# Performance work log

Hardware: AMD Instinct MI355X
Metric: run time of the kernel (lower is better)

Reference implementation:

```python
import jax, jax.numpy as jnp
import numpy as np

N = 100_000            # nodes
E = 1_600_000          # edges per metapath
IN = 256               # input features
HEADS, DIM = 8, 16     # heads * dim = hidden_channels
HIDDEN = HEADS * DIM   # 128
OUT = 4                # classes
NEG_SLOPE = 0.2


def setup_inputs() -> dict:
    key = jax.random.key(0)
    ks = jax.random.split(key, 16)
    s = 1.0 / np.sqrt(HIDDEN)
    return {
        "x": jax.random.normal(ks[0], (N, IN), jnp.float32),
        "edge_index0": jax.random.randint(ks[1], (2, E), 0, N, jnp.int64),
        "edge_index1": jax.random.randint(ks[2], (2, E), 0, N, jnp.int64),
        "proj_w": jax.random.normal(ks[3], (IN, HIDDEN), jnp.float32) / np.sqrt(IN),
        "proj_b": jnp.zeros((HIDDEN,), jnp.float32),
        "att_src0": jax.random.normal(ks[4], (HEADS, DIM), jnp.float32) * s,
        "att_dst0": jax.random.normal(ks[5], (HEADS, DIM), jnp.float32) * s,
        "att_src1": jax.random.normal(ks[6], (HEADS, DIM), jnp.float32) * s,
        "att_dst1": jax.random.normal(ks[7], (HEADS, DIM), jnp.float32) * s,
        "k_lin_w": jax.random.normal(ks[8], (HIDDEN, HIDDEN), jnp.float32) * s,
        "k_lin_b": jnp.zeros((HIDDEN,), jnp.float32),
        "q": jax.random.normal(ks[9], (HIDDEN,), jnp.float32) * s,
        "lin_w": jax.random.normal(ks[10], (HIDDEN, OUT), jnp.float32) * s,
        "lin_b": jnp.zeros((OUT,), jnp.float32),
    }


def _metapath_conv(xp, a_src, a_dst, src, dst):
    # xp: [N,H,D]; a_src, a_dst: [H,D]; src/dst: [E]
    alpha_src = (xp * a_src).sum(-1)                     # [N,H]
    alpha_dst = (xp * a_dst).sum(-1)                     # [N,H]
    e = jax.nn.leaky_relu(alpha_src[src] + alpha_dst[dst], NEG_SLOPE)  # [E,H]
    emax = jax.ops.segment_max(e, dst, num_segments=N)  # [N,H] (stable softmax)
    e = jnp.exp(e - emax[dst])
    denom = jax.ops.segment_sum(e, dst, num_segments=N)
    alpha = e / (denom[dst] + 1e-16)                     # edge softmax per dst
    msg = xp[src] * alpha[..., None]                     # [E,H,D]
    out = jax.ops.segment_sum(msg, dst, num_segments=N)  # [N,H,D]
    return jax.nn.relu(out.reshape(N, HIDDEN))


def reference(x, edge_index0, edge_index1, proj_w, proj_b,
              att_src0, att_dst0, att_src1, att_dst1,
              k_lin_w, k_lin_b, q, lin_w, lin_b):
    # shared node-type projection
    xp = (x @ proj_w + proj_b).reshape(N, HEADS, DIM)
    # per-metapath GAT-style convolutions (dropout=0.6 is eval no-op)
    outs = jnp.stack([
        _metapath_conv(xp, att_src0, att_dst0, edge_index0[0], edge_index0[1]),
        _metapath_conv(xp, att_src1, att_dst1, edge_index1[0], edge_index1[1]),
    ])                                                    # [M,N,HIDDEN]
    # semantic attention over metapaths
    k = jnp.tanh(outs @ k_lin_w + k_lin_b).mean(axis=1)  # [M,HIDDEN]
    attn = jax.nn.softmax((k * q).sum(-1))               # [M]
    fused = (attn[:, None, None] * outs).sum(0)          # [N,HIDDEN]
    return fused @ lin_w + lin_b                          # [N,OUT]
```

## Files before the change

kernel.cpp:

```cpp
#include <hip/hip_runtime.h>
#include <hip/hip_bf16.h>

#define NN 100000
#define EE 1600000
#define HID 128
#define NEG 0.2f
#define CAP 64
#define BSH 9
#define NB 196
#define CAPB 9216
#define EBLK 4096

typedef __attribute__((ext_vector_type(8))) short short8;
typedef __attribute__((ext_vector_type(4))) float f32x4;

#define PWS 264
#define PNT ((NN + 15) / 16)

__global__ __launch_bounds__(256) void k_proj(const float* __restrict__ x,
    const float* __restrict__ w, const float* __restrict__ bias,
    __hip_bfloat16* __restrict__ xph) {
  __shared__ short wT[128 * PWS];
  const int tid = threadIdx.x;
  for (int l = tid; l < 256 * 128; l += 256) {
    int k = l >> 7, n = l & 127;
    __hip_bfloat16 bv = __float2bfloat16(w[l]);
    wT[n * PWS + k] = *(short*)&bv;
  }
  const int lane = tid & 63, wave = tid >> 6;
  const int rowgrp = lane >> 4, lcol = lane & 15;
  float bv[8];
#pragma unroll
  for (int ct = 0; ct < 8; ct++) bv[ct] = bias[ct * 16 + lcol];
  __syncthreads();
  for (int tile = blockIdx.x * 4 + wave; tile < PNT; tile += gridDim.x * 4) {
    const int r0 = tile * 16;
    int row = r0 + lcol;
    if (row >= NN) row = NN - 1;
    const float* xr = x + (size_t)row * 256 + rowgrp * 8;
    short8 af[8];
#pragma unroll
    for (int kc = 0; kc < 8; kc++) {
      float4 u0 = *(const float4*)(xr + kc * 32);
      float4 u1 = *(const float4*)(xr + kc * 32 + 4);
      union { short8 v; __hip_bfloat162 h[4]; } u;
      u.h[0] = __float22bfloat162_rn(make_float2(u0.x, u0.y));
      u.h[1] = __float22bfloat162_rn(make_float2(u0.z, u0.w));
      u.h[2] = __float22bfloat162_rn(make_float2(u1.x, u1.y));
      u.h[3] = __float22bfloat162_rn(make_float2(u1.z, u1.w));
      af[kc] = u.v;
    }
#pragma unroll
    for (int ct = 0; ct < 8; ct++) {
      f32x4 acc = {0.f, 0.f, 0.f, 0.f};
#pragma unroll
      for (int kc = 0; kc < 8; kc++) {
        short8 bf = *(const short8*)&wT[(ct * 16 + lcol) * PWS + kc * 32 + rowgrp * 8];
        acc = __builtin_amdgcn_mfma_f32_16x16x32_bf16(af[kc], bf, acc, 0, 0, 0);
      }
#pragma unroll
      for (int r = 0; r < 4; r++) {
        int orow = r0 + rowgrp * 4 + r;
        if (orow < NN) {
          __hip_bfloat16 ob = __float2bfloat16(acc[r] + bv[ct]);
          ((short*)xph)[(size_t)orow * 128 + ct * 16 + lcol] = *(short*)&ob;
        }
      }
    }
  }
}

__global__ __launch_bounds__(256) void k_alpha(const __hip_bfloat162* __restrict__ xph,
    const float* __restrict__ a0s, const float* __restrict__ a0d,
    const float* __restrict__ a1s, const float* __restrict__ a1d,
    float* __restrict__ as0, float* __restrict__ ad0,
    float* __restrict__ as1, float* __restrict__ ad1) {
  const int lane = threadIdx.x & 63;
  const int node = blockIdx.x * 4 + (threadIdx.x >> 6);
  if (node >= NN) return;
  float2 v = __bfloat1622float2(xph[(size_t)node * 64 + lane]);
  int i0 = 2 * lane;
  float p0 = v.x * a0s[i0] + v.y * a0s[i0 + 1];
  float p1 = v.x * a0d[i0] + v.y * a0d[i0 + 1];
  float p2 = v.x * a1s[i0] + v.y * a1s[i0 + 1];
  float p3 = v.x * a1d[i0] + v.y * a1d[i0 + 1];
#pragma unroll
  for (int off = 1; off < 8; off <<= 1) {
    p0 += __shfl_xor(p0, off, 64);
    p1 += __shfl_xor(p1, off, 64);
    p2 += __shfl_xor(p2, off, 64);
    p3 += __shfl_xor(p3, off, 64);
  }
  if ((lane & 7) == 0) {
    int h = lane >> 3;
    as0[node * 8 + h] = p0;
    ad0[node * 8 + h] = p1;
    as1[node * 8 + h] = p2;
    ad1[node * 8 + h] = p3;
  }
}

__global__ __launch_bounds__(256) void k_bin(const int* __restrict__ ei0,
    const int* __restrict__ ei1, int* __restrict__ gcur, int* __restrict__ binned) {
  const int p = blockIdx.y;
  const int* __restrict__ ei = p ? ei1 : ei0;
  const int* __restrict__ src = ei;
  const int* __restrict__ dst = ei + EE;
  int* __restrict__ gc = gcur + p * 256;
  int* __restrict__ bn = binned + (size_t)p * NB * CAPB;
  __shared__ int cntL[NB], baseL[NB], posL[NB];
  const int t = threadIdx.x;
  const int e0 = blockIdx.x * EBLK;
  const int e1 = min(e0 + EBLK, EE);
  for (int i = t; i < NB; i += 256) { cntL[i] = 0; posL[i] = 0; }
  __syncthreads();
  for (int e = e0 + t; e < e1; e += 256)
    atomicAdd(&cntL[dst[e] >> BSH], 1);
  __syncthreads();
  for (int i = t; i < NB; i += 256)
    baseL[i] = atomicAdd(&gc[i], cntL[i]);
  __syncthreads();
  for (int e = e0 + t; e < e1; e += 256) {
    int d = dst[e];
    int b = d >> BSH;
    int off = baseL[b] + atomicAdd(&posL[b], 1);
    if (off < CAPB) bn[b * CAPB + off] = (src[e] << BSH) | (d & 511);
  }
}

__global__ __launch_bounds__(512) void k_build(const int* __restrict__ gcur,
    const int* __restrict__ binned, int* __restrict__ cnt, int* __restrict__ csr) {
  const int p = blockIdx.y, b = blockIdx.x, t = threadIdx.x;
  const int* __restrict__ bn = binned + (size_t)p * NB * CAPB + (size_t)b * CAPB;
  const int n = min(gcur[p * 256 + b], CAPB);
  int* __restrict__ cs = csr + (size_t)p * NN * CAP;
  __shared__ int lc[512];
  lc[t] = 0;
  __syncthreads();
  const int node0 = b << BSH;
  for (int i = t; i < n; i += 512) {
    int v = bn[i];
    int ln = v & 511;
    int off = atomicAdd(&lc[ln], 1);
    if (off < CAP) cs[(size_t)(node0 + ln) * CAP + off] = v >> BSH;
  }
  __syncthreads();
  int n0 = node0 + t;
  if (n0 < NN) cnt[p * NN + n0] = lc[t];
}

#define LRELU(t) ((t) > 0.f ? (t) : NEG * (t))

#define EDGE_BODY(sv)                                      \
  {                                                        \
    unsigned s = (unsigned)(sv);                           \
    float t = asrc[s * 8u + h];                            \
    __hip_bfloat162 v = xph[s * 64u + lane];               \
    float al = __expf(LRELU(t + ad));                      \
    denom += al;                                           \
    float2 f = __bfloat1622float2(v);                      \
    a0 = fmaf(al, f.x, a0);                                \
    a1 = fmaf(al, f.y, a1);                                \
  }

__global__ __launch_bounds__(256) void k_aggr(const __hip_bfloat162* __restrict__ xph,
    const float* __restrict__ as0, const float* __restrict__ ad0,
    const float* __restrict__ as1, const float* __restrict__ ad1,
    const int* __restrict__ cnt, const int* __restrict__ csr,
    __hip_bfloat162* __restrict__ h0, __hip_bfloat162* __restrict__ h1) {
  const int p = blockIdx.y;
  const unsigned lane = threadIdx.x & 63;
  const int node = blockIdx.x * 4 + (threadIdx.x >> 6);
  if (node >= NN) return;
  const float* __restrict__ asrc = p ? as1 : as0;
  const float* __restrict__ adst = p ? ad1 : ad0;
  const int* __restrict__ cs = csr + ((size_t)p * NN + node) * CAP;
  __hip_bfloat162* __restrict__ hout = p ? h1 : h0;
  const unsigned h = lane >> 3;
  const float ad = adst[(unsigned)node * 8u + h];
  const int deg = min(cnt[p * NN + node], CAP);

  float denom = 1e-16f, a0 = 0.f, a1 = 0.f;
  int e = 0;
  for (; e + 8 <= deg; e += 8) {
    int4 q0 = *(const int4*)&cs[e];
    int4 q1 = *(const int4*)&cs[e + 4];
    EDGE_BODY(q0.x) EDGE_BODY(q0.y) EDGE_BODY(q0.z) EDGE_BODY(q0.w)
    EDGE_BODY(q1.x) EDGE_BODY(q1.y) EDGE_BODY(q1.z) EDGE_BODY(q1.w)
  }
  for (; e + 4 <= deg; e += 4) {
    int4 q0 = *(const int4*)&cs[e];
    EDGE_BODY(q0.x) EDGE_BODY(q0.y) EDGE_BODY(q0.z) EDGE_BODY(q0.w)
  }
  for (; e < deg; e++) EDGE_BODY(cs[e])
  float inv = 1.f / denom;
  hout[(size_t)node * 64 + lane] =
      __float22bfloat162_rn(make_float2(fmaxf(a0 * inv, 0.f), fmaxf(a1 * inv, 0.f)));
}

#define KWS 136
#define NTILES ((NN + 63) / 64)
#define SEMGX 256

__global__ __launch_bounds__(256) void k_sem(const __hip_bfloat16* __restrict__ h0,
    const __hip_bfloat16* __restrict__ h1, const float* __restrict__ kw,
    const float* __restrict__ kb, float* __restrict__ ksum) {
  __shared__ short kwT[128 * KWS];
  __shared__ float red[4][128];
  const int tid = threadIdx.x;
  const int m = blockIdx.y;
  const short* __restrict__ hc = (const short*)(m ? h1 : h0);
  for (int l = tid; l < 128 * 128; l += 256) {
    int i = l >> 7, j = l & 127;
    __hip_bfloat16 bv = __float2bfloat16(kw[l]);
    kwT[j * KWS + i] = *(short*)&bv;
  }
  const int lane = tid & 63;
  const int wave = tid >> 6;
  const int rowgrp = lane >> 4;
  const int lcol = lane & 15;
  float partial[8] = {};
  float kbv[8];
#pragma unroll
  for (int ct = 0; ct < 8; ct++) kbv[ct] = kb[ct * 16 + lcol];
  __syncthreads();
  for (int tile = blockIdx.x; tile < NTILES; tile += SEMGX) {
    int n0 = tile * 64 + wave * 16;
    int row = n0 + lcol;
    if (row >= NN) row = 0;
    const short* hr = hc + (size_t)row * 128 + rowgrp * 8;
    short8 afrag[4];
#pragma unroll
    for (int kc = 0; kc < 4; kc++) afrag[kc] = *(const short8*)(hr + kc * 32);
#pragma unroll
    for (int ct = 0; ct < 8; ct++) {
      f32x4 acc = {0.f, 0.f, 0.f, 0.f};
#pragma unroll
      for (int kc = 0; kc < 4; kc++) {
        short8 bfrag = *(const short8*)&kwT[(ct * 16 + lcol) * KWS + kc * 32 + rowgrp * 8];
        acc = __builtin_amdgcn_mfma_f32_16x16x32_bf16(afrag[kc], bfrag, acc, 0, 0, 0);
      }
#pragma unroll
      for (int r = 0; r < 4; r++) {
        int node = n0 + rowgrp * 4 + r;
        if (node < NN) partial[ct] += tanhf(acc[r] + kbv[ct]);
      }
    }
  }
#pragma unroll
  for (int ct = 0; ct < 8; ct++) {
    partial[ct] += __shfl_xor(partial[ct], 16, 64);
    partial[ct] += __shfl_xor(partial[ct], 32, 64);
  }
  if (lane < 16) {
#pragma unroll
    for (int ct = 0; ct < 8; ct++) red[wave][ct * 16 + lane] = partial[ct];
  }
  __syncthreads();
  if (tid < 128) {
    float s = red[0][tid] + red[1][tid] + red[2][tid] + red[3][tid];
    atomicAdd(&ksum[m * 128 + tid], s);
  }
}

__global__ void k_attn(const float* __restrict__ ksum, const float* __restrict__ q,
                       float* __restrict__ attn) {
  __shared__ float red0[128], red1[128];
  int t = threadIdx.x;
  float qv = q[t];
  red0[t] = ksum[t] * qv;
  red1[t] = ksum[128 + t] * qv;
  __syncthreads();
  for (int off = 64; off > 0; off >>= 1) {
    if (t < off) {
      red0[t] += red0[t + off];
      red1[t] += red1[t + off];
    }
    __syncthreads();
  }
  if (t == 0) {
    float l0 = red0[0] / (float)NN, l1 = red1[0] / (float)NN;
    float mx = fmaxf(l0, l1);
    float e0 = __expf(l0 - mx), e1 = __expf(l1 - mx);
    float s = e0 + e1;
    attn[0] = e0 / s;
    attn[1] = e1 / s;
  }
}

__global__ __launch_bounds__(256) void k_final(const __hip_bfloat162* __restrict__ h0,
    const __hip_bfloat162* __restrict__ h1, const float* __restrict__ lw,
    const float* __restrict__ lb, const float* __restrict__ attn,
    float* __restrict__ out) {
  const int lane = threadIdx.x & 63;
  const int node = blockIdx.x * 4 + (threadIdx.x >> 6);
  if (node >= NN) return;
  float a0 = attn[0], a1 = attn[1];
  float2 v0 = __bfloat1622float2(h0[(size_t)node * 64 + lane]);
  float2 v1 = __bfloat1622float2(h1[(size_t)node * 64 + lane]);
  float f0 = a0 * v0.x + a1 * v1.x;
  float f1 = a0 * v0.y + a1 * v1.y;
  int i0 = 2 * lane;
  float p[4];
#pragma unroll
  for (int c = 0; c < 4; c++)
    p[c] = f0 * lw[i0 * 4 + c] + f1 * lw[(i0 + 1) * 4 + c];
#pragma unroll
  for (int off = 32; off > 0; off >>= 1) {
#pragma unroll
    for (int c = 0; c < 4; c++) p[c] += __shfl_down(p[c], off, 64);
  }
  if (lane == 0) {
#pragma unroll
    for (int c = 0; c < 4; c++) out[(size_t)node * 4 + c] = p[c] + lb[c];
  }
}

extern "C" void kernel_launch(void* const* d_in, const int* in_sizes, int n_in,
                              void* d_out, int out_size, void* d_ws, size_t ws_size,
                              hipStream_t stream) {
  const float* x      = (const float*)d_in[0];
  const int*   ei0    = (const int*)d_in[1];
  const int*   ei1    = (const int*)d_in[2];
  const float* proj_w = (const float*)d_in[3];
  const float* proj_b = (const float*)d_in[4];
  const float* a0s    = (const float*)d_in[5];
  const float* a0d    = (const float*)d_in[6];
  const float* a1s    = (const float*)d_in[7];
  const float* a1d    = (const float*)d_in[8];
  const float* klw    = (const float*)d_in[9];
  const float* klb    = (const float*)d_in[10];
  const float* q      = (const float*)d_in[11];
  const float* lw     = (const float*)d_in[12];
  const float* lb     = (const float*)d_in[13];
  float* out = (float*)d_out;

  char* ws = (char*)d_ws;
  size_t off = 0;
  auto alloc = [&](size_t bytes) -> void* {
    size_t o = (off + 255) & ~(size_t)255;
    off = o + bytes;
    return (void*)(ws + o);
  };
  __hip_bfloat162* xph = (__hip_bfloat162*)alloc((size_t)NN * 128 * 2);
  __hip_bfloat162* h0  = (__hip_bfloat162*)alloc((size_t)NN * 128 * 2);
  __hip_bfloat162* h1  = (__hip_bfloat162*)alloc((size_t)NN * 128 * 2);
  float* as0  = (float*)alloc((size_t)NN * 8 * 4);
  float* ad0  = (float*)alloc((size_t)NN * 8 * 4);
  float* as1  = (float*)alloc((size_t)NN * 8 * 4);
  float* ad1  = (float*)alloc((size_t)NN * 8 * 4);
  int* cnt    = (int*)alloc((size_t)2 * NN * 4);
  float* ksum = (float*)alloc(256 * 4);
  int* gcur   = (int*)alloc(2 * 256 * 4);
  float* attn = (float*)alloc(256);
  int* csr    = (int*)alloc((size_t)2 * NN * CAP * 4);
  int* binned = (int*)alloc((size_t)2 * NB * CAPB * 4);

  hipMemsetAsync(cnt, 0, (size_t)2 * NN * 4 + 256 * 4 + 2 * 256 * 4, stream);

  k_proj<<<dim3(256), 256, 0, stream>>>(x, proj_w, proj_b, (__hip_bfloat16*)xph);
  k_alpha<<<dim3((NN + 3) / 4), 256, 0, stream>>>(xph, a0s, a0d, a1s, a1d,
                                                  as0, ad0, as1, ad1);
  k_bin<<<dim3((EE + EBLK - 1) / EBLK, 2), 256, 0, stream>>>(ei0, ei1, gcur, binned);
  k_build<<<dim3(NB, 2), 512, 0, stream>>>(gcur, binned, cnt, csr);
  k_aggr<<<dim3((NN + 3) / 4, 2), 256, 0, stream>>>(xph, as0, ad0, as1, ad1,
                                                    cnt, csr, h0, h1);
  k_sem<<<dim3(SEMGX, 2), 256, 0, stream>>>((const __hip_bfloat16*)h0,
                                            (const __hip_bfloat16*)h1, klw, klb, ksum);
  k_attn<<<dim3(1), 128, 0, stream>>>(ksum, q, attn);
  k_final<<<dim3((NN + 3) / 4), 256, 0, stream>>>(h0, h1, lw, lb, attn, out);
}
```

Baseline: 528.4 us.

## Fuse attention logits into projection and output head into semantic kernel

The per-node attention scores are now computed inside the projection GEMM epilogue from fp32 accumulators, which removes the separate k_alpha pass over xph. The final linear head is applied per metapath inside k_sem, reusing the already-loaded h fragments, and a tiny blend kernel combines the two 4-wide outputs with the semantic weights. This avoids re-reading h0/h1 in a final kernel. The change also doubles the grid sizes of k_proj and k_sem, switches leaky-relu to a fmax form, and makes the node index wave-uniform in aggregation. The fused epilogue adds shuffle reductions per output tile, and alpha values now come from unrounded fp32 rather than bf16.

```diff
diff --git a/kernel.cpp b/kernel.cpp
--- a/kernel.cpp
+++ b/kernel.cpp
@@ -14,12 +14,23 @@
 typedef __attribute__((ext_vector_type(8))) short short8;
 typedef __attribute__((ext_vector_type(4))) float f32x4;
 
+static __device__ __forceinline__ float bf2f(short s) {
+  union { float f; unsigned u; } c;
+  c.u = ((unsigned)(unsigned short)s) << 16;
+  return c.f;
+}
+
 #define PWS 264
 #define PNT ((NN + 15) / 16)
+#define PGX 512
 
 __global__ __launch_bounds__(256) void k_proj(const float* __restrict__ x,
     const float* __restrict__ w, const float* __restrict__ bias,
-    __hip_bfloat16* __restrict__ xph) {
+    const float* __restrict__ a0s, const float* __restrict__ a0d,
+    const float* __restrict__ a1s, const float* __restrict__ a1d,
+    __hip_bfloat16* __restrict__ xph,
+    float* __restrict__ as0, float* __restrict__ ad0,
+    float* __restrict__ as1, float* __restrict__ ad1) {
   __shared__ short wT[128 * PWS];
   const int tid = threadIdx.x;
   for (int l = tid; l < 256 * 128; l += 256) {
@@ -29,9 +40,15 @@
   }
   const int lane = tid & 63, wave = tid >> 6;
   const int rowgrp = lane >> 4, lcol = lane & 15;
-  float bv[8];
-#pragma unroll
-  for (int ct = 0; ct < 8; ct++) bv[ct] = bias[ct * 16 + lcol];
+  float bv[8], A0S[8], A0D[8], A1S[8], A1D[8];
+#pragma unroll
+  for (int ct = 0; ct < 8; ct++) {
+    bv[ct] = bias[ct * 16 + lcol];
+    A0S[ct] = a0s[ct * 16 + lcol];
+    A0D[ct] = a0d[ct * 16 + lcol];
+    A1S[ct] = a1s[ct * 16 + lcol];
+    A1D[ct] = a1d[ct * 16 + lcol];
+  }
   __syncthreads();
   for (int tile = blockIdx.x * 4 + wave; tile < PNT; tile += gridDim.x * 4) {
     const int r0 = tile * 16;
@@ -61,42 +78,27 @@
 #pragma unroll
       for (int r = 0; r < 4; r++) {
         int orow = r0 + rowgrp * 4 + r;
+        float xv = acc[r] + bv[ct];
         if (orow < NN) {
-          __hip_bfloat16 ob = __float2bfloat16(acc[r] + bv[ct]);
+          __hip_bfloat16 ob = __float2bfloat16(xv);
           ((short*)xph)[(size_t)orow * 128 + ct * 16 + lcol] = *(short*)&ob;
         }
-      }
-    }
-  }
-}
-
-__global__ __launch_bounds__(256) void k_alpha(const __hip_bfloat162* __restrict__ xph,
-    const float* __restrict__ a0s, const float* __restrict__ a0d,
-    const float* __restrict__ a1s, const float* __restrict__ a1d,
-    float* __restrict__ as0, float* __restrict__ ad0,
-    float* __restrict__ as1, float* __restrict__ ad1) {
-  const int lane = threadIdx.x & 63;
-  const int node = blockIdx.x * 4 + (threadIdx.x >> 6);
-  if (node >= NN) return;
-  float2 v = __bfloat1622float2(xph[(size_t)node * 64 + lane]);
-  int i0 = 2 * lane;
-  float p0 = v.x * a0s[i0] + v.y * a0s[i0 + 1];
-  float p1 = v.x * a0d[i0] + v.y * a0d[i0 + 1];
-  float p2 = v.x * a1s[i0] + v.y * a1s[i0 + 1];
-  float p3 = v.x * a1d[i0] + v.y * a1d[i0 + 1];
-#pragma unroll
-  for (int off = 1; off < 8; off <<= 1) {
-    p0 += __shfl_xor(p0, off, 64);
-    p1 += __shfl_xor(p1, off, 64);
-    p2 += __shfl_xor(p2, off, 64);
-    p3 += __shfl_xor(p3, off, 64);
-  }
-  if ((lane & 7) == 0) {
-    int h = lane >> 3;
-    as0[node * 8 + h] = p0;
-    ad0[node * 8 + h] = p1;
-    as1[node * 8 + h] = p2;
-    ad1[node * 8 + h] = p3;
+        float q0 = xv * A0S[ct], q1 = xv * A0D[ct], q2 = xv * A1S[ct], q3 = xv * A1D[ct];
+#pragma unroll
+        for (int off = 1; off < 16; off <<= 1) {
+          q0 += __shfl_xor(q0, off, 64);
+          q1 += __shfl_xor(q1, off, 64);
+          q2 += __shfl_xor(q2, off, 64);
+          q3 += __shfl_xor(q3, off, 64);
+        }
+        if (lcol == 0 && orow < NN) {
+          as0[orow * 8 + ct] = q0;
+          ad0[orow * 8 + ct] = q1;
+          as1[orow * 8 + ct] = q2;
+          ad1[orow * 8 + ct] = q3;
+        }
+      }
+    }
   }
 }
 
@@ -149,14 +151,14 @@
   if (n0 < NN) cnt[p * NN + n0] = lc[t];
 }
 
-#define LRELU(t) ((t) > 0.f ? (t) : NEG * (t))
 
 #define EDGE_BODY(sv)                                      \
   {                                                        \
     unsigned s = (unsigned)(sv);                           \
     float t = asrc[s * 8u + h];                            \
     __hip_bfloat162 v = xph[s * 64u + lane];               \
-    float al = __expf(LRELU(t + ad));                      \
+    float tt = t + ad;                                     \
+    float al = __expf(fmaxf(tt, NEG * tt));                \
     denom += al;                                           \
     float2 f = __bfloat1622float2(v);                      \
     a0 = fmaf(al, f.x, a0);                                \
@@ -170,8 +172,9 @@
     __hip_bfloat162* __restrict__ h0, __hip_bfloat162* __restrict__ h1) {
   const int p = blockIdx.y;
   const unsigned lane = threadIdx.x & 63;
-  const int node = blockIdx.x * 4 + (threadIdx.x >> 6);
+  int node = blockIdx.x * 4 + (threadIdx.x >> 6);
   if (node >= NN) return;
+  node = __builtin_amdgcn_readfirstlane(node);
   const float* __restrict__ asrc = p ? as1 : as0;
   const float* __restrict__ adst = p ? ad1 : ad0;
   const int* __restrict__ cs = csr + ((size_t)p * NN + node) * CAP;
@@ -200,21 +203,25 @@
 
 #define KWS 136
 #define NTILES ((NN + 63) / 64)
-#define SEMGX 256
+#define SEMGX 512
 
 __global__ __launch_bounds__(256) void k_sem(const __hip_bfloat16* __restrict__ h0,
     const __hip_bfloat16* __restrict__ h1, const float* __restrict__ kw,
-    const float* __restrict__ kb, float* __restrict__ ksum) {
+    const float* __restrict__ kb, const float* __restrict__ lw,
+    float* __restrict__ ksum, float* __restrict__ o0, float* __restrict__ o1) {
   __shared__ short kwT[128 * KWS];
   __shared__ float red[4][128];
+  __shared__ float lwS[512];
   const int tid = threadIdx.x;
   const int m = blockIdx.y;
   const short* __restrict__ hc = (const short*)(m ? h1 : h0);
+  float* __restrict__ oc = m ? o1 : o0;
   for (int l = tid; l < 128 * 128; l += 256) {
     int i = l >> 7, j = l & 127;
     __hip_bfloat16 bv = __float2bfloat16(kw[l]);
     kwT[j * KWS + i] = *(short*)&bv;
   }
+  for (int l = tid; l < 512; l += 256) lwS[l] = lw[l];
   const int lane = tid & 63;
   const int wave = tid >> 6;
   const int rowgrp = lane >> 4;
@@ -232,6 +239,31 @@
     short8 afrag[4];
 #pragma unroll
     for (int kc = 0; kc < 4; kc++) afrag[kc] = *(const short8*)(hr + kc * 32);
+    float op[4] = {0.f, 0.f, 0.f, 0.f};
+#pragma unroll
+    for (int kc = 0; kc < 4; kc++) {
+      union { short8 v; short s[8]; } u;
+      u.v = afrag[kc];
+#pragma unroll
+      for (int j = 0; j < 8; j++) {
+        float hv = bf2f(u.s[j]);
+        const float4 lv = *(const float4*)&lwS[(kc * 32 + rowgrp * 8 + j) * 4];
+        op[0] = fmaf(hv, lv.x, op[0]);
+        op[1] = fmaf(hv, lv.y, op[1]);
+        op[2] = fmaf(hv, lv.z, op[2]);
+        op[3] = fmaf(hv, lv.w, op[3]);
+      }
+    }
+#pragma unroll
+    for (int c = 0; c < 4; c++) {
+      op[c] += __shfl_xor(op[c], 16, 64);
+      op[c] += __shfl_xor(op[c], 32, 64);
+    }
+    int orow = n0 + lcol;
+    if (rowgrp == 0 && orow < NN) {
+      float4 ov = make_float4(op[0], op[1], op[2], op[3]);
+      *(float4*)&oc[(size_t)orow * 4] = ov;
+    }
 #pragma unroll
     for (int ct = 0; ct < 8; ct++) {
       f32x4 acc = {0.f, 0.f, 0.f, 0.f};
@@ -288,32 +320,12 @@
   }
 }
 
-__global__ __launch_bounds__(256) void k_final(const __hip_bfloat162* __restrict__ h0,
-    const __hip_bfloat162* __restrict__ h1, const float* __restrict__ lw,
-    const float* __restrict__ lb, const float* __restrict__ attn,
-    float* __restrict__ out) {
-  const int lane = threadIdx.x & 63;
-  const int node = blockIdx.x * 4 + (threadIdx.x >> 6);
-  if (node >= NN) return;
-  float a0 = attn[0], a1 = attn[1];
-  float2 v0 = __bfloat1622float2(h0[(size_t)node * 64 + lane]);
-  float2 v1 = __bfloat1622float2(h1[(size_t)node * 64 + lane]);
-  float f0 = a0 * v0.x + a1 * v1.x;
-  float f1 = a0 * v0.y + a1 * v1.y;
-  int i0 = 2 * lane;
-  float p[4];
-#pragma unroll
-  for (int c = 0; c < 4; c++)
-    p[c] = f0 * lw[i0 * 4 + c] + f1 * lw[(i0 + 1) * 4 + c];
-#pragma unroll
-  for (int off = 32; off > 0; off >>= 1) {
-#pragma unroll
-    for (int c = 0; c < 4; c++) p[c] += __shfl_down(p[c], off, 64);
-  }
-  if (lane == 0) {
-#pragma unroll
-    for (int c = 0; c < 4; c++) out[(size_t)node * 4 + c] = p[c] + lb[c];
-  }
+__global__ __launch_bounds__(256) void k_blend(const float* __restrict__ o0,
+    const float* __restrict__ o1, const float* __restrict__ lb,
+    const float* __restrict__ attn, float* __restrict__ out) {
+  int i = blockIdx.x * 256 + threadIdx.x;
+  if (i >= NN * 4) return;
+  out[i] = attn[0] * o0[i] + attn[1] * o1[i] + lb[i & 3];
 }
 
 extern "C" void kernel_launch(void* const* d_in, const int* in_sizes, int n_in,
@@ -355,18 +367,20 @@
   float* attn = (float*)alloc(256);
   int* csr    = (int*)alloc((size_t)2 * NN * CAP * 4);
   int* binned = (int*)alloc((size_t)2 * NB * CAPB * 4);
+  float* o0   = (float*)alloc((size_t)NN * 4 * 4);
+  float* o1   = (float*)alloc((size_t)NN * 4 * 4);
 
   hipMemsetAsync(cnt, 0, (size_t)2 * NN * 4 + 256 * 4 + 2 * 256 * 4, stream);
 
-  k_proj<<<dim3(256), 256, 0, stream>>>(x, proj_w, proj_b, (__hip_bfloat16*)xph);
-  k_alpha<<<dim3((NN + 3) / 4), 256, 0, stream>>>(xph, a0s, a0d, a1s, a1d,
-                                                  as0, ad0, as1, ad1);
+  k_proj<<<dim3(PGX), 256, 0, stream>>>(x, proj_w, proj_b, a0s, a0d, a1s, a1d,
+                                        (__hip_bfloat16*)xph, as0, ad0, as1, ad1);
   k_bin<<<dim3((EE + EBLK - 1) / EBLK, 2), 256, 0, stream>>>(ei0, ei1, gcur, binned);
   k_build<<<dim3(NB, 2), 512, 0, stream>>>(gcur, binned, cnt, csr);
   k_aggr<<<dim3((NN + 3) / 4, 2), 256, 0, stream>>>(xph, as0, ad0, as1, ad1,
                                                     cnt, csr, h0, h1);
   k_sem<<<dim3(SEMGX, 2), 256, 0, stream>>>((const __hip_bfloat16*)h0,
-                                            (const __hip_bfloat16*)h1, klw, klb, ksum);
+                                            (const __hip_bfloat16*)h1, klw, klb, lw,
+                                            ksum, o0, o1);
   k_attn<<<dim3(1), 128, 0, stream>>>(ksum, q, attn);
-  k_final<<<dim3((NN + 3) / 4), 256, 0, stream>>>(h0, h1, lw, lb, attn, out);
-}
+  k_blend<<<dim3((NN * 4 + 255) / 256), 256, 0, stream>>>(o0, o1, lb, attn, out);
+}
```

New measurement: 526.4 us. About the same (-0.4%).
